# Kernel optimization log

Hardware: AMD Instinct MI355X
Metric: run time of the kernel (lower is better)

The kernel has to match this reference:

```python
import jax, jax.numpy as jnp
import numpy as np

B, N, K, D = 2, 4096, 20, 128
PH = 8          # pos_mlp hidden dim
AH = 4 * D      # attn_mlp hidden dim (attn_mlp_hidden_mult=4)


def setup_inputs() -> dict:
    key = jax.random.key(0)
    ks = jax.random.split(key, 12)
    s = 0.02
    f32 = jnp.float32
    return {
        "x": jax.random.normal(ks[0], (B, N, 3), f32),
        "pos": jax.random.normal(ks[1], (B, N, 3), f32),
        # linear1/2/3 (torch Linear: y = x @ W.T + b)
        "W1": jax.random.normal(ks[2], (D, 3), f32) * s,  "b1": jnp.zeros((D,), f32),
        "W2": jax.random.normal(ks[3], (D, D), f32) * s,  "b2": jnp.zeros((D,), f32),
        "W3": jax.random.normal(ks[4], (D, D), f32) * s,  "b3": jnp.zeros((D,), f32),
        # PointTransformerLayer params
        "Wqkv": jax.random.normal(ks[5], (3 * D, D), f32) * s,          # to_qkv, no bias
        "Wp1": jax.random.normal(ks[6], (PH, 3), f32) * s,  "bp1": jnp.zeros((PH,), f32),
        "Wp2": jax.random.normal(ks[7], (D, PH), f32) * s,  "bp2": jnp.zeros((D,), f32),
        "Wa1": jax.random.normal(ks[8], (AH, D), f32) * s,  "ba1": jnp.zeros((AH,), f32),
        "Wa2": jax.random.normal(ks[9], (D, AH), f32) * s,  "ba2": jnp.zeros((D,), f32),
    }


def reference(x, pos, W1, b1, W2, b2, W3, b3, Wqkv,
              Wp1, bp1, Wp2, bp2, Wa1, ba1, Wa2, ba2):
    h = x @ W1.T + b1            # [B,N,D] linear1
    h1 = h @ W2.T + b2           # [B,N,D] linear2

    # --- PointTransformerLayer (lucidrains, KNN vector attention) ---
    qkv = h1 @ Wqkv.T            # [B,N,3D]
    q, k, v = jnp.split(qkv, 3, axis=-1)

    # squared pairwise distances and K nearest neighbors (self included)
    d2 = jnp.sum((pos[:, :, None, :] - pos[:, None, :, :]) ** 2, axis=-1)  # [B,N,N]
    _, idx = jax.lax.top_k(-d2, K)                                          # [B,N,K]

    gather = jax.vmap(lambda arr, ind: arr[ind])  # per-batch gather -> [B,N,K,*]
    kn = gather(k, idx)          # [B,N,K,D]
    vn = gather(v, idx)          # [B,N,K,D]
    pn = gather(pos, idx)        # [B,N,K,3]

    rel = pos[:, :, None, :] - pn                                   # [B,N,K,3]
    pe = jax.nn.relu(rel @ Wp1.T + bp1) @ Wp2.T + bp2               # pos_mlp [B,N,K,D]

    vn = vn + pe
    sim = jax.nn.relu((q[:, :, None, :] - kn + pe) @ Wa1.T + ba1) @ Wa2.T + ba2  # attn_mlp
    attn = jax.nn.softmax(sim, axis=2)                              # softmax over neighbors
    agg = jnp.sum(attn * vn, axis=2)                                # [B,N,D]

    return h + (agg @ W3.T + b3)  # residual: x + linear3(x1)
```

## Files before the change

### kernel.cpp

```cpp
#include <hip/hip_runtime.h>
#include <stdint.h>

#define BB 2
#define NN 4096
#define KNB 20
#define DD 128
#define PHH 8
#define AHH 512
#define BN (BB*NN)

typedef unsigned short ushort_t;
typedef short bf16x8 __attribute__((ext_vector_type(8)));
typedef float f32x4 __attribute__((ext_vector_type(4)));

__device__ __forceinline__ uint32_t umin32(uint32_t a, uint32_t b) { return a < b ? a : b; }
__device__ __forceinline__ uint32_t umax32(uint32_t a, uint32_t b) { return a > b ? a : b; }

__device__ __forceinline__ float bf2f(ushort_t u) {
    union { float f; uint32_t i; } c; c.i = ((uint32_t)u) << 16; return c.f;
}
__device__ __forceinline__ uint32_t cvt_pk_bf16(float lo, float hi) {
    uint32_t r;
    asm("v_cvt_pk_bf16_f32 %0, %1, %2" : "=v"(r) : "v"(lo), "v"(hi));
    return r;
}
__device__ __forceinline__ ushort_t f2bf(float f) {
    return (ushort_t)(cvt_pk_bf16(f, f) & 0xFFFFu);
}
__device__ __forceinline__ bf16x8 load_bfrag(const float* __restrict__ src) {
    float4 x = *(const float4*)src;
    float4 y = *(const float4*)(src + 4);
    union { bf16x8 v; uint32_t u[4]; } r;
    r.u[0] = cvt_pk_bf16(x.x, x.y);
    r.u[1] = cvt_pk_bf16(x.z, x.w);
    r.u[2] = cvt_pk_bf16(y.x, y.y);
    r.u[3] = cvt_pk_bf16(y.z, y.w);
    return r.v;
}

#define SW256(m, byteInRow) ((m)*256 + ((byteInRow) ^ (((m)&7) << 4)))

__global__ __launch_bounds__(256) void k_prep(
        const float* __restrict__ Wa1f, const float* __restrict__ Wa2f,
        const float* __restrict__ Wp2f,
        ushort_t* __restrict__ Wa1bf, ushort_t* __restrict__ Wa2bf,
        ushort_t* __restrict__ Wfusebf) {
    int bid = blockIdx.x, tid = threadIdx.x;
    if (bid < 64) {
        int base = bid * 2048 + tid * 8;
        const float* src = (base < 65536) ? (Wa1f + base) : (Wa2f + (base - 65536));
        ushort_t* dst = (base < 65536) ? (Wa1bf + base) : (Wa2bf + (base - 65536));
        union { ushort_t u[8]; uint4 q; } pk;
        #pragma unroll
        for (int i = 0; i < 8; ++i) pk.u[i] = f2bf(src[i]);
        *(uint4*)dst = pk.q;
    } else {
        int a = (bid - 64) * 256 + tid;
        float s[PHH];
        #pragma unroll
        for (int jj = 0; jj < PHH; ++jj) s[jj] = 0.f;
        for (int d = 0; d < DD; ++d) {
            float wv = Wa1f[(size_t)a*DD + d];
            #pragma unroll
            for (int jj = 0; jj < PHH; ++jj) s[jj] += wv * Wp2f[d*PHH + jj];
        }
        union { ushort_t u[8]; uint4 q; } pk;
        #pragma unroll
        for (int jj = 0; jj < PHH; ++jj) pk.u[jj] = f2bf(s[jj]);
        *(uint4*)&Wfusebf[a*PHH] = pk.q;
    }
}

__global__ __launch_bounds__(256) void k_front(
        const float* __restrict__ x,
        const float* __restrict__ W1, const float* __restrict__ b1,
        const float* __restrict__ W2f, const float* __restrict__ b2,
        const float* __restrict__ Wqkvf,
        const ushort_t* __restrict__ Wa1bf, const float* __restrict__ ba1,
        float* __restrict__ h, ushort_t* __restrict__ vf,
        ushort_t* __restrict__ QWbf, ushort_t* __restrict__ KWbf) {
    __shared__ __align__(16) char smem[16896];
    float* xs = (float*)(smem + 16384);
    int tid = threadIdx.x, w = tid >> 6, lane = tid & 63;
    int lg = lane >> 4, c16 = lane & 15;
    int p0 = blockIdx.x * 32;

    if (tid < 96) xs[tid] = x[(size_t)p0*3 + tid];
    __syncthreads();

    #pragma unroll
    for (int it = 0; it < 16; ++it) {
        int lin = it*256 + tid;
        int m = lin >> 7, d = lin & 127;
        float hv = b1[d] + xs[m*3+0]*W1[d*3+0] + xs[m*3+1]*W1[d*3+1] + xs[m*3+2]*W1[d*3+2];
        h[(size_t)(p0+m)*DD + d] = hv;
        *(ushort_t*)&smem[SW256(m, d*2)] = f2bf(hv);
    }
    __syncthreads();

    {
        f32x4 acc[2][2];
        #pragma unroll
        for (int mt = 0; mt < 2; ++mt)
            #pragma unroll
            for (int ntl = 0; ntl < 2; ++ntl) acc[mt][ntl] = (f32x4){0,0,0,0};
        #pragma unroll
        for (int ks = 0; ks < 4; ++ks) {
            int k0 = ks*32 + lg*8;
            bf16x8 aF[2];
            #pragma unroll
            for (int mt = 0; mt < 2; ++mt)
                aF[mt] = *(const bf16x8*)&smem[SW256(mt*16 + c16, k0*2)];
            #pragma unroll
            for (int ntl = 0; ntl < 2; ++ntl) {
                int n = (2*w + ntl)*16 + c16;
                bf16x8 bF = load_bfrag(W2f + (size_t)n*DD + k0);
                #pragma unroll
                for (int mt = 0; mt < 2; ++mt)
                    acc[mt][ntl] = __builtin_amdgcn_mfma_f32_16x16x32_bf16(aF[mt], bF, acc[mt][ntl], 0, 0, 0);
            }
        }
        #pragma unroll
        for (int ntl = 0; ntl < 2; ++ntl) {
            int n = (2*w + ntl)*16 + c16;
            float bias = b2[n];
            #pragma unroll
            for (int mt = 0; mt < 2; ++mt)
                #pragma unroll
                for (int i = 0; i < 4; ++i) {
                    int m = mt*16 + lg*4 + i;
                    *(ushort_t*)&smem[8192 + SW256(m, n*2)] = f2bf(acc[mt][ntl][i] + bias);
                }
        }
    }
    __syncthreads();

    {
        f32x4 acc[2][6];
        #pragma unroll
        for (int mt = 0; mt < 2; ++mt)
            #pragma unroll
            for (int ntl = 0; ntl < 6; ++ntl) acc[mt][ntl] = (f32x4){0,0,0,0};
        #pragma unroll
        for (int ks = 0; ks < 4; ++ks) {
            int k0 = ks*32 + lg*8;
            bf16x8 aF[2];
            #pragma unroll
            for (int mt = 0; mt < 2; ++mt)
                aF[mt] = *(const bf16x8*)&smem[8192 + SW256(mt*16 + c16, k0*2)];
            #pragma unroll
            for (int ntl = 0; ntl < 6; ++ntl) {
                int n = (w*6 + ntl)*16 + c16;
                bf16x8 bF = load_bfrag(Wqkvf + (size_t)n*DD + k0);
                #pragma unroll
                for (int mt = 0; mt < 2; ++mt)
                    acc[mt][ntl] = __builtin_amdgcn_mfma_f32_16x16x32_bf16(aF[mt], bF, acc[mt][ntl], 0, 0, 0);
            }
        }
        #pragma unroll
        for (int ntl = 0; ntl < 6; ++ntl) {
            int n = (w*6 + ntl)*16 + c16;
            int r = n >> 7, d = n & 127;
            #pragma unroll
            for (int mt = 0; mt < 2; ++mt)
                #pragma unroll
                for (int i = 0; i < 4; ++i) {
                    int m = mt*16 + lg*4 + i;
                    if (r == 0) *(ushort_t*)&smem[SW256(m, d*2)] = f2bf(acc[mt][ntl][i]);
                    else if (r == 2) vf[(size_t)(p0+m)*DD + d] = f2bf(acc[mt][ntl][i]);
                }
        }
        __syncthreads();
        #pragma unroll
        for (int ntl = 0; ntl < 6; ++ntl) {
            int n = (w*6 + ntl)*16 + c16;
            int r = n >> 7, d = n & 127;
            if (r == 1) {
                #pragma unroll
                for (int mt = 0; mt < 2; ++mt)
                    #pragma unroll
                    for (int i = 0; i < 4; ++i) {
                        int m = mt*16 + lg*4 + i;
                        *(ushort_t*)&smem[8192 + SW256(m, d*2)] = f2bf(acc[mt][ntl][i]);
                    }
            }
        }
    }
    __syncthreads();

    #pragma unroll
    for (int half = 0; half < 2; ++half) {
        f32x4 accQ[2][4], accK[2][4];
        #pragma unroll
        for (int mt = 0; mt < 2; ++mt)
            #pragma unroll
            for (int ntl = 0; ntl < 4; ++ntl) {
                accQ[mt][ntl] = (f32x4){0,0,0,0};
                accK[mt][ntl] = (f32x4){0,0,0,0};
            }
        #pragma unroll
        for (int ks = 0; ks < 4; ++ks) {
            int k0 = ks*32 + lg*8;
            bf16x8 aQ[2], aK[2];
            #pragma unroll
            for (int mt = 0; mt < 2; ++mt) {
                aQ[mt] = *(const bf16x8*)&smem[SW256(mt*16 + c16, k0*2)];
                aK[mt] = *(const bf16x8*)&smem[8192 + SW256(mt*16 + c16, k0*2)];
            }
            #pragma unroll
            for (int ntl = 0; ntl < 4; ++ntl) {
                int n = (w*8 + half*4 + ntl)*16 + c16;
                bf16x8 bF = *(const bf16x8*)&Wa1bf[(size_t)n*DD + k0];
                #pragma unroll
                for (int mt = 0; mt < 2; ++mt) {
                    accQ[mt][ntl] = __builtin_amdgcn_mfma_f32_16x16x32_bf16(aQ[mt], bF, accQ[mt][ntl], 0, 0, 0);
                    accK[mt][ntl] = __builtin_amdgcn_mfma_f32_16x16x32_bf16(aK[mt], bF, accK[mt][ntl], 0, 0, 0);
                }
            }
        }
        #pragma unroll
        for (int ntl = 0; ntl < 4; ++ntl) {
            int n = (w*8 + half*4 + ntl)*16 + c16;
            float bias = ba1[n];
            #pragma unroll
            for (int mt = 0; mt < 2; ++mt)
                #pragma unroll
                for (int i = 0; i < 4; ++i) {
                    int m = mt*16 + lg*4 + i;
                    QWbf[(size_t)(p0+m)*AHH + n] = f2bf(accQ[mt][ntl][i] + bias);
                    KWbf[(size_t)(p0+m)*AHH + n] = f2bf(accK[mt][ntl][i]);
                }
        }
    }
}

__global__ __launch_bounds__(256) void k_knn(const float* __restrict__ pos, int* __restrict__ idx) {
    int wid  = threadIdx.x >> 6;
    int lane = threadIdx.x & 63;
    int p = blockIdx.x*4 + wid;
    int b = p >> 12;
    float qx = pos[p*3+0], qy = pos[p*3+1], qz = pos[p*3+2];
    const float* pb = pos + (size_t)b*NN*3;

    uint32_t bk[KNB];
    #pragma unroll
    for (int i = 0; i < KNB; ++i) bk[i] = 0xFFFFFFFFu;

    for (int i = 0; i < NN/64; ++i) {
        int j = i*64 + lane;
        float dx = qx - pb[j*3+0];
        float dy = qy - pb[j*3+1];
        float dz = qz - pb[j*3+2];
        float d2 = dx*dx + dy*dy + dz*dz;
        uint32_t key = (__float_as_uint(d2) & 0xFFFFF000u) | (uint32_t)j;
        if (key < bk[KNB-1]) {
            uint32_t c = key;
            #pragma unroll
            for (int t = 0; t < KNB; ++t) {
                uint32_t lo = umin32(c, bk[t]);
                uint32_t hi = umax32(c, bk[t]);
                bk[t] = lo; c = hi;
            }
        }
    }
    for (int r = 0; r < KNB; ++r) {
        uint32_t m = bk[0];
        #pragma unroll
        for (int s = 1; s < 64; s <<= 1)
            m = umin32(m, (uint32_t)__shfl_xor((int)m, s, 64));
        if (lane == 0) idx[(size_t)p*KNB + r] = (int)(m & 0xFFFu);
        bool win = (bk[0] == m);
        #pragma unroll
        for (int t = 0; t < KNB-1; ++t) bk[t] = win ? bk[t+1] : bk[t];
        bk[KNB-1] = win ? 0xFFFFFFFFu : bk[KNB-1];
    }
}

#define TL_OFF 0
#define PH_OFF 20480
#define NIDX_OFF 21760

__global__ __launch_bounds__(256, 4) void k_attn(
        const float* __restrict__ pos,
        const ushort_t* __restrict__ QWbf, const ushort_t* __restrict__ KWbf,
        const ushort_t* __restrict__ vf, const int* __restrict__ idx,
        const float* __restrict__ Wp1, const float* __restrict__ bp1,
        const float* __restrict__ Wp2, const float* __restrict__ bp2,
        const ushort_t* __restrict__ Wfusebf,
        const ushort_t* __restrict__ Wa2bf, const float* __restrict__ ba2,
        float* __restrict__ agg) {
    __shared__ __align__(16) char smem[22080];
    int* nidx = (int*)(smem + NIDX_OFF);

    int tid = threadIdx.x, w = tid >> 6, lane = tid & 63;
    int lg = lane >> 4, c16 = lane & 15;
    int bid = blockIdx.x;
    int xcd = bid & 7, sloc = bid >> 3;
    int b = xcd >> 2;
    int p0 = b*NN + ((xcd & 3)*256 + sloc)*4;

    if (tid < 80) nidx[tid] = idx[(size_t)(p0 + tid/20)*KNB + (tid%20)];
    __syncthreads();

    if (tid < 80) {
        int m = tid, g = m / 20;
        int j = nidx[m];
        const float* pq = pos + (size_t)(p0+g)*3;
        const float* pn = pos + (size_t)(b*NN+j)*3;
        float r0 = pq[0]-pn[0], r1 = pq[1]-pn[1], r2 = pq[2]-pn[2];
        union { ushort_t u[8]; uint4 q; } pk;
        #pragma unroll
        for (int jj = 0; jj < PHH; ++jj) {
            float a = bp1[jj] + r0*Wp1[jj*3+0] + r1*Wp1[jj*3+1] + r2*Wp1[jj*3+2];
            pk.u[jj] = f2bf(fmaxf(a, 0.f));
        }
        *(uint4*)&smem[PH_OFF + m*16] = pk.q;
    }
    __syncthreads();

    int dA = w*32 + 2*c16, dB = dA + 1;
    float bp2A = bp2[dA], bp2B = bp2[dB];
    float ba2A = ba2[dA], ba2B = ba2[dB];

    bf16x8 bP0 = {0,0,0,0,0,0,0,0}, bP1 = {0,0,0,0,0,0,0,0};
    if (lg == 0) {
        bP0 = load_bfrag(Wp2 + (size_t)dA*PHH);
        bP1 = load_bfrag(Wp2 + (size_t)dB*PHH);
    }
    uint32_t vpe_pk[5][4];
    #pragma unroll
    for (int mt = 0; mt < 5; ++mt) {
        bf16x8 aP = {0,0,0,0,0,0,0,0};
        if (lg == 0) aP = *(const bf16x8*)&smem[PH_OFF + (mt*16 + c16)*16];
        f32x4 accP0 = (f32x4){0,0,0,0}, accP1 = (f32x4){0,0,0,0};
        accP0 = __builtin_amdgcn_mfma_f32_16x16x32_bf16(aP, bP0, accP0, 0, 0, 0);
        accP1 = __builtin_amdgcn_mfma_f32_16x16x32_bf16(aP, bP1, accP1, 0, 0, 0);
        #pragma unroll
        for (int i = 0; i < 4; ++i) {
            int m = mt*16 + lg*4 + i;
            int j = nidx[m];
            uint32_t vw = *(const uint32_t*)&vf[(size_t)(b*NN+j)*DD + dA];
            float peA = accP0[i] + bp2A;
            float peB = accP1[i] + bp2B;
            vpe_pk[mt][i] = cvt_pk_bf16(bf2f((ushort_t)(vw & 0xFFFFu)) + peA,
                                        bf2f((ushort_t)(vw >> 16)) + peB);
        }
    }

    f32x4 accS[5][2];
    #pragma unroll
    for (int mt = 0; mt < 5; ++mt)
        #pragma unroll
        for (int ntl = 0; ntl < 2; ++ntl) accS[mt][ntl] = (f32x4){0,0,0,0};

    for (int c = 0; c < 4; ++c) {
        int aQ0 = c*128 + dA;
        bf16x8 bF0 = {0,0,0,0,0,0,0,0}, bF1 = {0,0,0,0,0,0,0,0};
        if (lg == 0) {
            bF0 = *(const bf16x8*)&Wfusebf[(size_t)aQ0*PHH];
            bF1 = *(const bf16x8*)&Wfusebf[(size_t)(aQ0+1)*PHH];
        }
        uint32_t qww[4];
        #pragma unroll
        for (int g = 0; g < 4; ++g)
            qww[g] = *(const uint32_t*)&QWbf[(size_t)(p0+g)*AHH + aQ0];
        uint32_t kwn[4];
        #pragma unroll
        for (int i = 0; i < 4; ++i)
            kwn[i] = *(const uint32_t*)&KWbf[(size_t)(b*NN + nidx[lg*4 + i])*AHH + aQ0];
        #pragma unroll
        for (int mt = 0; mt < 5; ++mt) {
            uint32_t kwc[4];
            #pragma unroll
            for (int i = 0; i < 4; ++i) kwc[i] = kwn[i];
            if (mt < 4) {
                #pragma unroll
                for (int i = 0; i < 4; ++i)
                    kwn[i] = *(const uint32_t*)&KWbf[(size_t)(b*NN + nidx[(mt+1)*16 + lg*4 + i])*AHH + aQ0];
            }
            bf16x8 aP = {0,0,0,0,0,0,0,0};
            if (lg == 0) aP = *(const bf16x8*)&smem[PH_OFF + (mt*16 + c16)*16];
            f32x4 accF0 = (f32x4){0,0,0,0}, accF1 = (f32x4){0,0,0,0};
            accF0 = __builtin_amdgcn_mfma_f32_16x16x32_bf16(aP, bF0, accF0, 0, 0, 0);
            accF1 = __builtin_amdgcn_mfma_f32_16x16x32_bf16(aP, bF1, accF1, 0, 0, 0);
            uint32_t qsel = (mt==0) ? qww[0]
                          : (mt==1) ? (lg>=1 ? qww[1] : qww[0])
                          : (mt==2) ? (lg>=2 ? qww[2] : qww[1])
                          : (mt==3) ? (lg==3 ? qww[3] : qww[2])
                          : qww[3];
            float qA = bf2f((ushort_t)(qsel & 0xFFFFu));
            float qB = bf2f((ushort_t)(qsel >> 16));
            #pragma unroll
            for (int i = 0; i < 4; ++i) {
                int m = mt*16 + lg*4 + i;
                float kA = bf2f((ushort_t)(kwc[i] & 0xFFFFu));
                float kB = bf2f((ushort_t)(kwc[i] >> 16));
                float tA = fmaxf(qA - kA + accF0[i], 0.f);
                float tB = fmaxf(qB - kB + accF1[i], 0.f);
                *(uint32_t*)&smem[TL_OFF + SW256(m, dA*2)] = cvt_pk_bf16(tA, tB);
            }
        }
        __syncthreads();

        __builtin_amdgcn_s_setprio(1);
        #pragma unroll
        for (int ks = 0; ks < 4; ++ks) {
            int k0 = ks*32 + lg*8;
            bf16x8 aF[5];
            #pragma unroll
            for (int mt = 0; mt < 5; ++mt)
                aF[mt] = *(const bf16x8*)&smem[TL_OFF + SW256(mt*16 + c16, k0*2)];
            bf16x8 bW0 = *(const bf16x8*)&Wa2bf[(size_t)dA*AHH + c*128 + k0];
            bf16x8 bW1 = *(const bf16x8*)&Wa2bf[(size_t)dB*AHH + c*128 + k0];
            #pragma unroll
            for (int mt = 0; mt < 5; ++mt) {
                accS[mt][0] = __builtin_amdgcn_mfma_f32_16x16x32_bf16(aF[mt], bW0, accS[mt][0], 0, 0, 0);
                accS[mt][1] = __builtin_amdgcn_mfma_f32_16x16x32_bf16(aF[mt], bW1, accS[mt][1], 0, 0, 0);
            }
        }
        __builtin_amdgcn_s_setprio(0);
        __syncthreads();
    }

    float s_mtA[5], a_mtA[5], s_mtB[5], a_mtB[5];
    #pragma unroll
    for (int mt = 0; mt < 5; ++mt) {
        float sa = 0.f, aa = 0.f, sb = 0.f, ab = 0.f;
        #pragma unroll
        for (int i = 0; i < 4; ++i) {
            float eA = __expf(accS[mt][0][i] + ba2A);
            float eB = __expf(accS[mt][1][i] + ba2B);
            uint32_t pk = vpe_pk[mt][i];
            float vA = bf2f((ushort_t)(pk & 0xFFFFu));
            float vB = bf2f((ushort_t)(pk >> 16));
            sa += eA; aa += eA*vA;
            sb += eB; ab += eB*vB;
        }
        s_mtA[mt] = sa; a_mtA[mt] = aa; s_mtB[mt] = sb; a_mtB[mt] = ab;
    }
    bool eq0 = (lg==0), ge1 = (lg>=1), ge2 = (lg>=2), le1 = (lg<=1), le2 = (lg<=2), eq3 = (lg==3);
    float s0A = s_mtA[0] + (eq0 ? s_mtA[1] : 0.f);
    float s1A = (ge1 ? s_mtA[1] : 0.f) + (le1 ? s_mtA[2] : 0.f);
    float s2A = (ge2 ? s_mtA[2] : 0.f) + (le2 ? s_mtA[3] : 0.f);
    float s3A = (eq3 ? s_mtA[3] : 0.f) + s_mtA[4];
    float a0A = a_mtA[0] + (eq0 ? a_mtA[1] : 0.f);
    float a1A = (ge1 ? a_mtA[1] : 0.f) + (le1 ? a_mtA[2] : 0.f);
    float a2A = (ge2 ? a_mtA[2] : 0.f) + (le2 ? a_mtA[3] : 0.f);
    float a3A = (eq3 ? a_mtA[3] : 0.f) + a_mtA[4];
    float s0B = s_mtB[0] + (eq0 ? s_mtB[1] : 0.f);
    float s1B = (ge1 ? s_mtB[1] : 0.f) + (le1 ? s_mtB[2] : 0.f);
    float s2B = (ge2 ? s_mtB[2] : 0.f) + (le2 ? s_mtB[3] : 0.f);
    float s3B = (eq3 ? s_mtB[3] : 0.f) + s_mtB[4];
    float a0B = a_mtB[0] + (eq0 ? a_mtB[1] : 0.f);
    float a1B = (ge1 ? a_mtB[1] : 0.f) + (le1 ? a_mtB[2] : 0.f);
    float a2B = (ge2 ? a_mtB[2] : 0.f) + (le2 ? a_mtB[3] : 0.f);
    float a3B = (eq3 ? a_mtB[3] : 0.f) + a_mtB[4];

    #define RED2(v) { v += __shfl_xor(v, 16, 64); v += __shfl_xor(v, 32, 64); }
    RED2(s0A) RED2(s1A) RED2(s2A) RED2(s3A)
    RED2(a0A) RED2(a1A) RED2(a2A) RED2(a3A)
    RED2(s0B) RED2(s1B) RED2(s2B) RED2(s3B)
    RED2(a0B) RED2(a1B) RED2(a2B) RED2(a3B)
    #undef RED2

    float myS_A = (lg==0) ? s0A : (lg==1) ? s1A : (lg==2) ? s2A : s3A;
    float myA_A = (lg==0) ? a0A : (lg==1) ? a1A : (lg==2) ? a2A : a3A;
    float myS_B = (lg==0) ? s0B : (lg==1) ? s1B : (lg==2) ? s2B : s3B;
    float myA_B = (lg==0) ? a0B : (lg==1) ? a1B : (lg==2) ? a2B : a3B;
    float2 st;
    st.x = myA_A / myS_A;
    st.y = myA_B / myS_B;
    *(float2*)&agg[(size_t)(p0+lg)*DD + dA] = st;
}

__global__ __launch_bounds__(256) void k_out(
        const float* __restrict__ agg, const float* __restrict__ h,
        const float* __restrict__ W3f, const float* __restrict__ b3,
        float* __restrict__ out) {
    __shared__ __align__(16) char smem[8192];
    int tid = threadIdx.x, w = tid >> 6, lane = tid & 63;
    int p0 = blockIdx.x * 32;

    #pragma unroll
    for (int it = 0; it < 16; ++it) {
        int lin = it*256 + tid;
        int m = lin >> 7, d = lin & 127;
        *(ushort_t*)&smem[SW256(m, d*2)] = f2bf(agg[(size_t)(p0+m)*DD + d]);
    }
    __syncthreads();

    f32x4 acc[2][2];
    #pragma unroll
    for (int mt = 0; mt < 2; ++mt)
        #pragma unroll
        for (int ntl = 0; ntl < 2; ++ntl) acc[mt][ntl] = (f32x4){0,0,0,0};
    #pragma unroll
    for (int ks = 0; ks < 4; ++ks) {
        int k0 = ks*32 + (lane >> 4)*8;
        bf16x8 aF[2];
        #pragma unroll
        for (int mt = 0; mt < 2; ++mt)
            aF[mt] = *(const bf16x8*)&smem[SW256(mt*16 + (lane & 15), k0*2)];
        #pragma unroll
        for (int ntl = 0; ntl < 2; ++ntl) {
            int n = (2*w + ntl)*16 + (lane & 15);
            bf16x8 bF = load_bfrag(W3f + (size_t)n*DD + k0);
            #pragma unroll
            for (int mt = 0; mt < 2; ++mt)
                acc[mt][ntl] = __builtin_amdgcn_mfma_f32_16x16x32_bf16(aF[mt], bF, acc[mt][ntl], 0, 0, 0);
        }
    }
    #pragma unroll
    for (int ntl = 0; ntl < 2; ++ntl) {
        int n = (2*w + ntl)*16 + (lane & 15);
        float bias = b3[n];
        #pragma unroll
        for (int mt = 0; mt < 2; ++mt)
            #pragma unroll
            for (int i = 0; i < 4; ++i) {
                int m = mt*16 + (lane >> 4)*4 + i;
                size_t o = (size_t)(p0+m)*DD + n;
                out[o] = acc[mt][ntl][i] + bias + h[o];
            }
    }
}

extern "C" void kernel_launch(void* const* d_in, const int* in_sizes, int n_in,
                              void* d_out, int out_size, void* d_ws, size_t ws_size,
                              hipStream_t stream) {
    const float* x    = (const float*)d_in[0];
    const float* pos  = (const float*)d_in[1];
    const float* W1   = (const float*)d_in[2];
    const float* b1   = (const float*)d_in[3];
    const float* W2   = (const float*)d_in[4];
    const float* b2   = (const float*)d_in[5];
    const float* W3   = (const float*)d_in[6];
    const float* b3   = (const float*)d_in[7];
    const float* Wqkv = (const float*)d_in[8];
    const float* Wp1  = (const float*)d_in[9];
    const float* bp1  = (const float*)d_in[10];
    const float* Wp2  = (const float*)d_in[11];
    const float* bp2  = (const float*)d_in[12];
    const float* Wa1  = (const float*)d_in[13];
    const float* ba1  = (const float*)d_in[14];
    const float* Wa2  = (const float*)d_in[15];
    const float* ba2  = (const float*)d_in[16];

    char* W = (char*)d_ws;
    float*    h       = (float*)(W + 0);
    float*    agg     = (float*)(W + 4194304);
    ushort_t* vf      = (ushort_t*)(W + 8388608);
    ushort_t* QWbf    = (ushort_t*)(W + 10485760);
    ushort_t* KWbf    = (ushort_t*)(W + 18874368);
    int*      idx     = (int*)(W + 27262976);
    ushort_t* Wa1bf   = (ushort_t*)(W + 27918336);
    ushort_t* Wa2bf   = (ushort_t*)(W + 28049408);
    ushort_t* Wfusebf = (ushort_t*)(W + 28180480);

    k_prep <<<66, 256, 0, stream>>>(Wa1, Wa2, Wp2, Wa1bf, Wa2bf, Wfusebf);
    k_front<<<BN/32, 256, 0, stream>>>(x, W1, b1, W2, b2, Wqkv, Wa1bf, ba1,
                                       h, vf, QWbf, KWbf);
    k_knn  <<<BN/4, 256, 0, stream>>>(pos, idx);
    k_attn <<<BN/4, 256, 0, stream>>>(pos, QWbf, KWbf, vf, idx,
                                      Wp1, bp1, Wp2, bp2, Wfusebf, Wa2bf, ba2, agg);
    k_out  <<<BN/32, 256, 0, stream>>>(agg, h, W3, b3, (float*)d_out);
}
```

Measured before the change: 165.3 us.

## Transpose positions to SoA for KNN and prefetch next-chunk QW/KW gathers in attention

The prep kernel gains extra blocks that transpose pos into a structure-of-arrays buffer, so the KNN scan can read float4 vectors of x, y and z with coalesced loads instead of stride-3 scalar loads. The attention kernel precomputes the neighbor row offsets and issues the gathered QW/KW loads for the next 128-wide chunk while the current chunk's Wa2 MFMAs run, hiding gather latency. This costs more live registers (about 40 extra uint32 values plus 20 size_t offsets), which could lower occupancy. It also adds a small extra workspace buffer and a little more work in the prep kernel.

Result: slower. 203.2 us (+22.9%).

```diff
diff --git a/kernel.cpp b/kernel.cpp
--- a/kernel.cpp
+++ b/kernel.cpp
@@ -42,9 +42,9 @@
 
 __global__ __launch_bounds__(256) void k_prep(
         const float* __restrict__ Wa1f, const float* __restrict__ Wa2f,
-        const float* __restrict__ Wp2f,
+        const float* __restrict__ Wp2f, const float* __restrict__ pos,
         ushort_t* __restrict__ Wa1bf, ushort_t* __restrict__ Wa2bf,
-        ushort_t* __restrict__ Wfusebf) {
+        ushort_t* __restrict__ Wfusebf, float* __restrict__ psoa) {
     int bid = blockIdx.x, tid = threadIdx.x;
     if (bid < 64) {
         int base = bid * 2048 + tid * 8;
@@ -54,7 +54,7 @@
         #pragma unroll
         for (int i = 0; i < 8; ++i) pk.u[i] = f2bf(src[i]);
         *(uint4*)dst = pk.q;
-    } else {
+    } else if (bid < 66) {
         int a = (bid - 64) * 256 + tid;
         float s[PHH];
         #pragma unroll
@@ -68,6 +68,19 @@
         #pragma unroll
         for (int jj = 0; jj < PHH; ++jj) pk.u[jj] = f2bf(s[jj]);
         *(uint4*)&Wfusebf[a*PHH] = pk.q;
+    } else {
+        int e0 = (bid - 66) * 2048 + tid * 8;
+        float v[8];
+        #pragma unroll
+        for (int i = 0; i < 8; ++i) {
+            int el = e0 + i;
+            int comp = el >> 13;
+            int rem = el & 8191;
+            v[i] = pos[(size_t)rem*3 + comp];
+        }
+        #pragma unroll
+        for (int i = 0; i < 8; i += 4)
+            *(float4*)&psoa[e0 + i] = (float4){v[i], v[i+1], v[i+2], v[i+3]};
     }
 }
 
@@ -234,32 +247,40 @@
     }
 }
 
-__global__ __launch_bounds__(256) void k_knn(const float* __restrict__ pos, int* __restrict__ idx) {
+__global__ __launch_bounds__(256) void k_knn(const float* __restrict__ pos,
+                                             const float* __restrict__ psoa,
+                                             int* __restrict__ idx) {
     int wid  = threadIdx.x >> 6;
     int lane = threadIdx.x & 63;
     int p = blockIdx.x*4 + wid;
     int b = p >> 12;
     float qx = pos[p*3+0], qy = pos[p*3+1], qz = pos[p*3+2];
-    const float* pb = pos + (size_t)b*NN*3;
+    const float4* px4 = (const float4*)(psoa + (size_t)b*NN);
+    const float4* py4 = (const float4*)(psoa + 8192 + (size_t)b*NN);
+    const float4* pz4 = (const float4*)(psoa + 16384 + (size_t)b*NN);
 
     uint32_t bk[KNB];
     #pragma unroll
     for (int i = 0; i < KNB; ++i) bk[i] = 0xFFFFFFFFu;
 
-    for (int i = 0; i < NN/64; ++i) {
-        int j = i*64 + lane;
-        float dx = qx - pb[j*3+0];
-        float dy = qy - pb[j*3+1];
-        float dz = qz - pb[j*3+2];
-        float d2 = dx*dx + dy*dy + dz*dz;
-        uint32_t key = (__float_as_uint(d2) & 0xFFFFF000u) | (uint32_t)j;
-        if (key < bk[KNB-1]) {
-            uint32_t c = key;
-            #pragma unroll
-            for (int t = 0; t < KNB; ++t) {
-                uint32_t lo = umin32(c, bk[t]);
-                uint32_t hi = umax32(c, bk[t]);
-                bk[t] = lo; c = hi;
+    for (int it = 0; it < NN/256; ++it) {
+        int j4 = it*64 + lane;
+        float4 X = px4[j4], Y = py4[j4], Z = pz4[j4];
+        #pragma unroll
+        for (int c = 0; c < 4; ++c) {
+            float dx = qx - ((c==0)?X.x:(c==1)?X.y:(c==2)?X.z:X.w);
+            float dy = qy - ((c==0)?Y.x:(c==1)?Y.y:(c==2)?Y.z:Y.w);
+            float dz = qz - ((c==0)?Z.x:(c==1)?Z.y:(c==2)?Z.z:Z.w);
+            float d2 = dx*dx + dy*dy + dz*dz;
+            uint32_t key = (__float_as_uint(d2) & 0xFFFFF000u) | (uint32_t)(j4*4 + c);
+            if (key < bk[KNB-1]) {
+                uint32_t cc = key;
+                #pragma unroll
+                for (int t = 0; t < KNB; ++t) {
+                    uint32_t lo = umin32(cc, bk[t]);
+                    uint32_t hi = umax32(cc, bk[t]);
+                    bk[t] = lo; cc = hi;
+                }
             }
         }
     }
@@ -322,6 +343,13 @@
     float bp2A = bp2[dA], bp2B = bp2[dB];
     float ba2A = ba2[dA], ba2B = ba2[dB];
 
+    size_t kwrow[5][4];
+    #pragma unroll
+    for (int mt = 0; mt < 5; ++mt)
+        #pragma unroll
+        for (int i = 0; i < 4; ++i)
+            kwrow[mt][i] = (size_t)(b*NN + nidx[mt*16 + lg*4 + i])*AHH;
+
     bf16x8 bP0 = {0,0,0,0,0,0,0,0}, bP1 = {0,0,0,0,0,0,0,0};
     if (lg == 0) {
         bP0 = load_bfrag(Wp2 + (size_t)dA*PHH);
@@ -353,6 +381,18 @@
         #pragma unroll
         for (int ntl = 0; ntl < 2; ++ntl) accS[mt][ntl] = (f32x4){0,0,0,0};
 
+    uint32_t qw_c[4], kw_c[5][4];
+    {
+        #pragma unroll
+        for (int g = 0; g < 4; ++g)
+            qw_c[g] = *(const uint32_t*)&QWbf[(size_t)(p0+g)*AHH + dA];
+        #pragma unroll
+        for (int mt = 0; mt < 5; ++mt)
+            #pragma unroll
+            for (int i = 0; i < 4; ++i)
+                kw_c[mt][i] = *(const uint32_t*)&KWbf[kwrow[mt][i] + dA];
+    }
+
     for (int c = 0; c < 4; ++c) {
         int aQ0 = c*128 + dA;
         bf16x8 bF0 = {0,0,0,0,0,0,0,0}, bF1 = {0,0,0,0,0,0,0,0};
@@ -360,47 +400,44 @@
             bF0 = *(const bf16x8*)&Wfusebf[(size_t)aQ0*PHH];
             bF1 = *(const bf16x8*)&Wfusebf[(size_t)(aQ0+1)*PHH];
         }
-        uint32_t qww[4];
-        #pragma unroll
-        for (int g = 0; g < 4; ++g)
-            qww[g] = *(const uint32_t*)&QWbf[(size_t)(p0+g)*AHH + aQ0];
-        uint32_t kwn[4];
-        #pragma unroll
-        for (int i = 0; i < 4; ++i)
-            kwn[i] = *(const uint32_t*)&KWbf[(size_t)(b*NN + nidx[lg*4 + i])*AHH + aQ0];
         #pragma unroll
         for (int mt = 0; mt < 5; ++mt) {
-            uint32_t kwc[4];
-            #pragma unroll
-            for (int i = 0; i < 4; ++i) kwc[i] = kwn[i];
-            if (mt < 4) {
-                #pragma unroll
-                for (int i = 0; i < 4; ++i)
-                    kwn[i] = *(const uint32_t*)&KWbf[(size_t)(b*NN + nidx[(mt+1)*16 + lg*4 + i])*AHH + aQ0];
-            }
             bf16x8 aP = {0,0,0,0,0,0,0,0};
             if (lg == 0) aP = *(const bf16x8*)&smem[PH_OFF + (mt*16 + c16)*16];
             f32x4 accF0 = (f32x4){0,0,0,0}, accF1 = (f32x4){0,0,0,0};
             accF0 = __builtin_amdgcn_mfma_f32_16x16x32_bf16(aP, bF0, accF0, 0, 0, 0);
             accF1 = __builtin_amdgcn_mfma_f32_16x16x32_bf16(aP, bF1, accF1, 0, 0, 0);
-            uint32_t qsel = (mt==0) ? qww[0]
-                          : (mt==1) ? (lg>=1 ? qww[1] : qww[0])
-                          : (mt==2) ? (lg>=2 ? qww[2] : qww[1])
-                          : (mt==3) ? (lg==3 ? qww[3] : qww[2])
-                          : qww[3];
+            uint32_t qsel = (mt==0) ? qw_c[0]
+                          : (mt==1) ? (lg>=1 ? qw_c[1] : qw_c[0])
+                          : (mt==2) ? (lg>=2 ? qw_c[2] : qw_c[1])
+                          : (mt==3) ? (lg==3 ? qw_c[3] : qw_c[2])
+                          : qw_c[3];
             float qA = bf2f((ushort_t)(qsel & 0xFFFFu));
             float qB = bf2f((ushort_t)(qsel >> 16));
             #pragma unroll
             for (int i = 0; i < 4; ++i) {
                 int m = mt*16 + lg*4 + i;
-                float kA = bf2f((ushort_t)(kwc[i] & 0xFFFFu));
-                float kB = bf2f((ushort_t)(kwc[i] >> 16));
+                float kA = bf2f((ushort_t)(kw_c[mt][i] & 0xFFFFu));
+                float kB = bf2f((ushort_t)(kw_c[mt][i] >> 16));
                 float tA = fmaxf(qA - kA + accF0[i], 0.f);
                 float tB = fmaxf(qB - kB + accF1[i], 0.f);
                 *(uint32_t*)&smem[TL_OFF + SW256(m, dA*2)] = cvt_pk_bf16(tA, tB);
             }
         }
         __syncthreads();
+
+        uint32_t qw_n[4], kw_n[5][4];
+        if (c < 3) {
+            int aQn = (c+1)*128 + dA;
+            #pragma unroll
+            for (int g = 0; g < 4; ++g)
+                qw_n[g] = *(const uint32_t*)&QWbf[(size_t)(p0+g)*AHH + aQn];
+            #pragma unroll
+            for (int mt = 0; mt < 5; ++mt)
+                #pragma unroll
+                for (int i = 0; i < 4; ++i)
+                    kw_n[mt][i] = *(const uint32_t*)&KWbf[kwrow[mt][i] + aQn];
+        }
 
         __builtin_amdgcn_s_setprio(1);
         #pragma unroll
@@ -420,6 +457,15 @@
         }
         __builtin_amdgcn_s_setprio(0);
         __syncthreads();
+
+        if (c < 3) {
+            #pragma unroll
+            for (int g = 0; g < 4; ++g) qw_c[g] = qw_n[g];
+            #pragma unroll
+            for (int mt = 0; mt < 5; ++mt)
+                #pragma unroll
+                for (int i = 0; i < 4; ++i) kw_c[mt][i] = kw_n[mt][i];
+        }
     }
 
     float s_mtA[5], a_mtA[5], s_mtB[5], a_mtB[5];
@@ -556,11 +602,12 @@
     ushort_t* Wa1bf   = (ushort_t*)(W + 27918336);
     ushort_t* Wa2bf   = (ushort_t*)(W + 28049408);
     ushort_t* Wfusebf = (ushort_t*)(W + 28180480);
-
-    k_prep <<<66, 256, 0, stream>>>(Wa1, Wa2, Wp2, Wa1bf, Wa2bf, Wfusebf);
+    float*    psoa    = (float*)(W + 28188672);
+
+    k_prep <<<78, 256, 0, stream>>>(Wa1, Wa2, Wp2, pos, Wa1bf, Wa2bf, Wfusebf, psoa);
     k_front<<<BN/32, 256, 0, stream>>>(x, W1, b1, W2, b2, Wqkv, Wa1bf, ba1,
                                        h, vf, QWbf, KWbf);
-    k_knn  <<<BN/4, 256, 0, stream>>>(pos, idx);
+    k_knn  <<<BN/4, 256, 0, stream>>>(pos, psoa, idx);
     k_attn <<<BN/4, 256, 0, stream>>>(pos, QWbf, KWbf, vf, idx,
                                       Wp1, bp1, Wp2, bp2, Wfusebf, Wa2bf, ba2, agg);
     k_out  <<<BN/32, 256, 0, stream>>>(agg, h, W3, b3, (float*)d_out);
```
